# Kernel optimization log

Measured on AMD Instinct MI355X. Metric: run time of the kernel, lower is better.

## Reference

```python
import math
import jax, jax.numpy as jnp
import numpy as np

BSZ, SEQ, DIM = 2, 2048, 4096
N_HEADS, N_KV = 32, 8
HEAD_DIM = DIM // N_HEADS  # 128
N_REP = N_HEADS // N_KV    # 4
EPS = 1e-5
ROPE_THETA = 500000.0


def setup_inputs() -> dict:
    key = jax.random.key(0)
    ks = jax.random.split(key, 6)
    scale = 0.02
    x = jax.random.normal(ks[0], (BSZ, SEQ, DIM), dtype=jnp.float32)
    wq = jax.random.normal(ks[1], (N_HEADS * HEAD_DIM, DIM), dtype=jnp.float32) * scale
    wk = jax.random.normal(ks[2], (N_KV * HEAD_DIM, DIM), dtype=jnp.float32) * scale
    wv = jax.random.normal(ks[3], (N_KV * HEAD_DIM, DIM), dtype=jnp.float32) * scale
    wo = jax.random.normal(ks[4], (N_HEADS * HEAD_DIM, DIM), dtype=jnp.float32).T * scale  # [DIM, n_heads*hd] -> stored as [out,in]
    wo = jax.random.normal(ks[4], (DIM, N_HEADS * HEAD_DIM), dtype=jnp.float32) * scale
    # RoPE tables (real/imag parts of freqs_cis)
    inv_freq = 1.0 / (ROPE_THETA ** (jnp.arange(0, HEAD_DIM, 2, dtype=jnp.float32) / HEAD_DIM))
    angles = jnp.arange(SEQ, dtype=jnp.float32)[:, None] * inv_freq[None, :]  # [SEQ, HEAD_DIM//2]
    cos, sin = jnp.cos(angles), jnp.sin(angles)
    # causal additive mask
    neg_inf = jnp.finfo(jnp.float32).min
    mask = jnp.where(jnp.tril(jnp.ones((SEQ, SEQ), dtype=bool)), 0.0, neg_inf).astype(jnp.float32)
    return {"x": x, "wq": wq, "wk": wk, "wv": wv, "wo": wo,
            "cos": cos, "sin": sin, "mask": mask, "start_pos": 0}


def _apply_rope(t, cos, sin):
    # t: [b, s, h, hd]; pairs (even, odd) as in view_as_complex
    tf = t.astype(jnp.float32).reshape(*t.shape[:-1], HEAD_DIM // 2, 2)
    e, o = tf[..., 0], tf[..., 1]
    c = cos[None, :, None, :]
    s = sin[None, :, None, :]
    out = jnp.stack([e * c - o * s, e * s + o * c], axis=-1)
    return out.reshape(t.shape).astype(t.dtype)


def _rmsnorm(t):
    tf = t.astype(jnp.float32)
    return (tf * jax.lax.rsqrt(jnp.mean(tf * tf, axis=-1, keepdims=True) + EPS)).astype(t.dtype)


def reference(x, wq, wk, wv, wo, cos, sin, mask, start_pos):
    b, s, _ = x.shape
    xq = (x @ wq.T).reshape(b, s, N_HEADS, HEAD_DIM)
    xk = (x @ wk.T).reshape(b, s, N_KV, HEAD_DIM)
    xv = (x @ wv.T).reshape(b, s, N_KV, HEAD_DIM)
    xq = _apply_rope(xq, cos, sin)
    xk = _apply_rope(xk, cos, sin)
    xq = _rmsnorm(xq)
    xk = _rmsnorm(xk)
    # KV cache write/read with start_pos=0 over seqlen tokens is identity here.
    # GQA without repeat_interleave: q head h attends kv head h // N_REP
    q = xq.transpose(0, 2, 1, 3).reshape(b, N_KV, N_REP, s, HEAD_DIM)
    k = xk.transpose(0, 2, 1, 3)  # [b, n_kv, s, hd]
    v = xv.transpose(0, 2, 1, 3)
    scale = 1.0 / math.sqrt(HEAD_DIM)
    scores = jnp.einsum('bgrqd,bgkd->bgrqk', q, k) * scale + mask[None, None, None]
    probs = jax.nn.softmax(scores, axis=-1)
    out = jnp.einsum('bgrqk,bgkd->bgrqd', probs, v)
    out = out.reshape(b, N_HEADS, s, HEAD_DIM).transpose(0, 2, 1, 3).reshape(b, s, N_HEADS * HEAD_DIM)
    return out @ wo.T
```

## Files before the change

### kernel.cpp

```cpp
#include <hip/hip_runtime.h>
#include <hip/hip_bf16.h>
#include <stdint.h>

#define SEQ 2048
#define DIMSZ 4096
#define QKVN 6144

typedef __attribute__((ext_vector_type(8))) __bf16 bf16x8;
typedef __attribute__((ext_vector_type(4))) float f32x4;

static __device__ __forceinline__ void gld_lds16(const void* g, void* l) {
  __builtin_amdgcn_global_load_lds(
      (__attribute__((address_space(1))) void*)(g),
      (__attribute__((address_space(3))) void*)(l), 16, 0, 0);
}

__global__ __launch_bounds__(256) void k_cvt5(const float* __restrict__ x,
                                              const float* __restrict__ wq,
                                              const float* __restrict__ wk,
                                              const float* __restrict__ wv,
                                              const float* __restrict__ wo,
                                              __bf16* __restrict__ xb,
                                              __bf16* __restrict__ wqkvb,
                                              __bf16* __restrict__ wob) {
  long vid = (long)blockIdx.x * 256 + threadIdx.x;
  const long stride = (long)gridDim.x * 256;
  for (; vid < 7340032L; vid += stride) {
    const float* src; __bf16* dst; long off;
    if (vid < 2097152L)      { src = x;  dst = xb;                off = vid; }
    else if (vid < 4194304L) { src = wq; dst = wqkvb;             off = vid - 2097152L; }
    else if (vid < 4718592L) { src = wk; dst = wqkvb + 16777216L; off = vid - 4194304L; }
    else if (vid < 5242880L) { src = wv; dst = wqkvb + 20971520L; off = vid - 4718592L; }
    else                     { src = wo; dst = wob;               off = vid - 5242880L; }
    const long e = off * 8;
    float4 v0 = *(const float4*)(src + e);
    float4 v1 = *(const float4*)(src + e + 4);
    bf16x8 o;
    o[0] = (__bf16)v0.x; o[1] = (__bf16)v0.y; o[2] = (__bf16)v0.z; o[3] = (__bf16)v0.w;
    o[4] = (__bf16)v1.x; o[5] = (__bf16)v1.y; o[6] = (__bf16)v1.z; o[7] = (__bf16)v1.w;
    *(bf16x8*)(dst + e) = o;
  }
}

template <typename OutT>
__global__ __launch_bounds__(512) void k_gemm8p(const __bf16* __restrict__ A,
                                                const __bf16* __restrict__ B,
                                                OutT* __restrict__ C,
                                                int M, int N, int K) {
  __shared__ __align__(16) __bf16 As[2][2][128 * 64];
  __shared__ __align__(16) __bf16 Bs[2][2][128 * 64];
  const int t = threadIdx.x;
  const int l = t & 63;
  const int w = t >> 6;
  const int wm = w >> 2;
  const int wn = w & 3;
  const int lr = l & 15, lg = l >> 4;
  const int sw = lr & 7;
  const int bm = blockIdx.y, bn = blockIdx.x;

  const int srow = t >> 3;
  const int scol = ((t & 7) ^ (srow & 7)) << 3;
  const __bf16* pa0 = A + (size_t)(bm * 256 +   0 + srow) * K + scol;
  const __bf16* pa1 = A + (size_t)(bm * 256 +  64 + srow) * K + scol;
  const __bf16* pa2 = A + (size_t)(bm * 256 + 128 + srow) * K + scol;
  const __bf16* pa3 = A + (size_t)(bm * 256 + 192 + srow) * K + scol;
  const __bf16* pb0 = B + (size_t)(bn * 256 +   0 + srow) * K + scol;
  const __bf16* pb1 = B + (size_t)(bn * 256 +  64 + srow) * K + scol;
  const __bf16* pb2 = B + (size_t)(bn * 256 + 128 + srow) * K + scol;
  const __bf16* pb3 = B + (size_t)(bn * 256 + 192 + srow) * K + scol;
  const int ldst = t * 8;

#define SA0(buf, kc) { gld_lds16(pa0 + (kc), &As[buf][0][ldst]); gld_lds16(pa1 + (kc), &As[buf][0][4096 + ldst]); }
#define SA1(buf, kc) { gld_lds16(pa2 + (kc), &As[buf][1][ldst]); gld_lds16(pa3 + (kc), &As[buf][1][4096 + ldst]); }
#define SB0(buf, kc) { gld_lds16(pb0 + (kc), &Bs[buf][0][ldst]); gld_lds16(pb1 + (kc), &Bs[buf][0][4096 + ldst]); }
#define SB1(buf, kc) { gld_lds16(pb2 + (kc), &Bs[buf][1][ldst]); gld_lds16(pb3 + (kc), &Bs[buf][1][4096 + ldst]); }

  const int c0 = ((lg ^ sw) * 8);
  const int c1 = (((lg ^ sw) ^ 4) * 8);
  const int aRow = lr;
  const int bRow = (wn & 1) * 64 + lr;

#define RDA(mi0, cur)                                                          \
  _Pragma("unroll") for (int mi = 0; mi < 4; ++mi) {                           \
    a[mi][0] = *(const bf16x8*)&As[cur][wm][(((mi0) + mi) * 16 + aRow) * 64 + c0]; \
    a[mi][1] = *(const bf16x8*)&As[cur][wm][(((mi0) + mi) * 16 + aRow) * 64 + c1]; \
  }
#define RDB(bv, ni0, cur)                                                      \
  _Pragma("unroll") for (int ni = 0; ni < 2; ++ni) {                           \
    bv[ni][0] = *(const bf16x8*)&Bs[cur][wn >> 1][(((ni0) + ni) * 16 + bRow) * 64 + c0]; \
    bv[ni][1] = *(const bf16x8*)&Bs[cur][wn >> 1][(((ni0) + ni) * 16 + bRow) * 64 + c1]; \
  }
#define PHTOP()                                        \
  asm volatile("" ::: "memory");                       \
  __builtin_amdgcn_s_barrier();                        \
  asm volatile("s_waitcnt lgkmcnt(0)" ::: "memory");   \
  __builtin_amdgcn_s_setprio(1)
#define PHEND()                                        \
  __builtin_amdgcn_s_setprio(0);                       \
  asm volatile("" ::: "memory");                       \
  __builtin_amdgcn_s_barrier()
#define PHENDW()                                       \
  __builtin_amdgcn_s_setprio(0);                       \
  asm volatile("s_waitcnt vmcnt(8)" ::: "memory");     \
  __builtin_amdgcn_s_barrier()
#define MMA16(am0, bv, ni0)                                                    \
  _Pragma("unroll") for (int mi = 0; mi < 4; ++mi)                             \
  _Pragma("unroll") for (int ni = 0; ni < 2; ++ni)                             \
  _Pragma("unroll") for (int kk = 0; kk < 2; ++kk)                             \
    acc[(am0) + mi][(ni0) + ni] = __builtin_amdgcn_mfma_f32_16x16x32_bf16(     \
        a[mi][kk], bv[ni][kk], acc[(am0) + mi][(ni0) + ni], 0, 0, 0);

  f32x4 acc[8][4] = {};
  const int nt = K >> 6;
  const int niter = nt >> 1;

  {
    const int k1 = (nt > 1 ? 1 : 0) << 6;
    SB0(0, 0); SB1(0, 0); SA0(0, 0); SA1(0, 0);
    SB0(1, k1); SB1(1, k1); SA0(1, k1); SA1(1, k1);
  }
  asm volatile("s_waitcnt vmcnt(8)" ::: "memory");
  asm volatile("" ::: "memory");
  __builtin_amdgcn_s_barrier();
  asm volatile("" ::: "memory");

  for (int i = 0; i < niter; ++i) {
    const int k2 = (2 * i + 2 < nt ? 2 * i + 2 : nt - 1) << 6;
    const int k3 = (2 * i + 3 < nt ? 2 * i + 3 : nt - 1) << 6;
    bf16x8 a[4][2], b0[2][2], b1[2][2];

    RDA(0, 0); RDB(b0, 0, 0);
    PHTOP(); MMA16(0, b0, 0); PHEND();
    RDB(b1, 2, 0);
    PHTOP(); MMA16(0, b1, 2); PHEND();
    RDA(4, 0);
    SB0(0, k2); SB1(0, k2);
    PHTOP(); MMA16(4, b1, 2); PHEND();
    SA0(0, k2); SA1(0, k2);
    PHTOP(); MMA16(4, b0, 0); PHENDW();

    RDA(0, 1); RDB(b0, 0, 1);
    PHTOP(); MMA16(0, b0, 0); PHEND();
    RDB(b1, 2, 1);
    PHTOP(); MMA16(0, b1, 2); PHEND();
    RDA(4, 1);
    SB0(1, k3); SB1(1, k3);
    PHTOP(); MMA16(4, b1, 2); PHEND();
    SA0(1, k3); SA1(1, k3);
    PHTOP(); MMA16(4, b0, 0); PHENDW();
  }
#undef SA0
#undef SA1
#undef SB0
#undef SB1
#undef RDA
#undef RDB
#undef PHTOP
#undef PHEND
#undef PHENDW
#undef MMA16

  const int row0 = bm * 256 + wm * 128;
  const int col0 = bn * 256 + wn * 64;
#pragma unroll
  for (int mi = 0; mi < 8; ++mi)
#pragma unroll
    for (int ni = 0; ni < 4; ++ni)
#pragma unroll
      for (int r = 0; r < 4; ++r)
        C[(size_t)(row0 + mi * 16 + lg * 4 + r) * N + (col0 + ni * 16 + lr)] =
            (OutT)acc[mi][ni][r];
}

__global__ __launch_bounds__(256) void k_rope_norm(__bf16* __restrict__ qkv,
                                                   const float* __restrict__ cosT,
                                                   const float* __restrict__ sinT) {
  const int task = blockIdx.x * 4 + (threadIdx.x >> 6);
  const int l = threadIdx.x & 63;
  const int m = task / 40;
  const int h = task - m * 40;
  const int s = m & (SEQ - 1);
  const bool isQ = h < 32;
  const int col = isQ ? h * 128 : 4096 + (h - 32) * 128;
  __bf16* p = qkv + (size_t)m * QKVN + col + l * 2;
  float e = (float)p[0], o = (float)p[1];
  float c = cosT[s * 64 + l], sn = sinT[s * 64 + l];
  float e2 = e * c - o * sn;
  float o2 = e * sn + o * c;
  float ss = e2 * e2 + o2 * o2;
#pragma unroll
  for (int off = 32; off > 0; off >>= 1) ss += __shfl_xor(ss, off);
  float r = rsqrtf(ss * (1.0f / 128.0f) + 1e-5f);
  if (isQ) r *= 0.08838834764831845f;
  p[0] = (__bf16)(e2 * r);
  p[1] = (__bf16)(o2 * r);
}

__global__ __launch_bounds__(256) void k_transpose_v(const __bf16* __restrict__ qkv,
                                                     __bf16* __restrict__ vt) {
  __shared__ __bf16 tile[64][136];
  const int t = threadIdx.x;
  const int st = blockIdx.x, bg = blockIdx.y;
  const int b = bg >> 3, g = bg & 7;
  const int s0 = st * 64;
#pragma unroll
  for (int p = 0; p < 4; ++p) {
    int row = p * 16 + (t >> 4);
    int co = (t & 15) * 8;
    *(bf16x8*)&tile[row][co] =
        *(const bf16x8*)&qkv[(size_t)(b * SEQ + s0 + row) * QKVN + 5120 + g * 128 + co];
  }
  __syncthreads();
#pragma unroll
  for (int p = 0; p < 4; ++p) {
    int d = p * 32 + (t >> 3);
    int so = (t & 7) * 8;
    bf16x8 v;
#pragma unroll
    for (int j = 0; j < 8; ++j) v[j] = tile[so + j][d];
    *(bf16x8*)&vt[((size_t)bg * 128 + d) * SEQ + s0 + so] = v;
  }
}

__global__ __launch_bounds__(256) void k_flash(const __bf16* __restrict__ qkv,
                                               const __bf16* __restrict__ vt,
                                               __bf16* __restrict__ attno) {
  __shared__ __bf16 Ks[64 * 128];
  __shared__ __bf16 Vs[128 * 64];
  __shared__ __bf16 Ps[4][16 * 64];
  const int t = threadIdx.x, w = t >> 6, l = t & 63;
  const int lr = l & 15, lg = l >> 4;
  const int bh = blockIdx.y;
  const int b = bh >> 5, h = bh & 31, g = h >> 2;
  const int qt0 = blockIdx.x, qt1 = 31 - (int)blockIdx.x;

  const __bf16* kp = qkv + 4096 + (size_t)(b * SEQ + (t >> 4)) * QKVN + g * 128 +
                     (((t & 15) ^ ((t >> 4) & 7)) * 8);
  const __bf16* vp = vt + (size_t)(b * 8 + g) * 128 * SEQ + (size_t)(t >> 3) * SEQ +
                     (((t & 7) ^ ((t >> 3) & 7)) * 8);
  const int wbase = (t & ~63) * 8;
  const int sw = lr & 7;

  for (int pass = 0; pass < 2; ++pass) {
    const int qt = (pass == 0) ? qt0 : qt1;

    const __bf16* Qb = qkv + (size_t)(b * SEQ + qt * 64 + w * 16 + lr) * QKVN + h * 128;
    bf16x8 qf[4];
#pragma unroll
    for (int kk = 0; kk < 4; ++kk) qf[kk] = *(const bf16x8*)&Qb[kk * 32 + lg * 8];

    f32x4 oacc[8] = {};
    float mrow[4], lsum[4];
#pragma unroll
    for (int r = 0; r < 4; ++r) { mrow[r] = -1e30f; lsum[r] = 0.f; }

    for (int kt = 0; kt <= qt; ++kt) {
      const size_t kv0 = (size_t)kt * 64;
#pragma unroll
      for (int i = 0; i < 4; ++i)
        gld_lds16(kp + (kv0 + i * 16) * QKVN, &Ks[i * 2048 + wbase]);
#pragma unroll
      for (int i = 0; i < 4; ++i)
        gld_lds16(vp + (size_t)i * 32 * SEQ + kv0, &Vs[i * 2048 + wbase]);
      __syncthreads();

      f32x4 sc[4] = {};
      __builtin_amdgcn_s_setprio(1);
#pragma unroll
      for (int kk = 0; kk < 4; ++kk)
#pragma unroll
        for (int n = 0; n < 4; ++n) {
          bf16x8 kf = *(const bf16x8*)&Ks[(n * 16 + lr) * 128 + ((kk * 4 + lg) ^ sw) * 8];
          sc[n] = __builtin_amdgcn_mfma_f32_16x16x32_bf16(qf[kk], kf, sc[n], 0, 0, 0);
        }
      __builtin_amdgcn_s_setprio(0);

      if (kt == qt) {
#pragma unroll
        for (int n = 0; n < 4; ++n)
#pragma unroll
          for (int r = 0; r < 4; ++r)
            if (n * 16 + lr > w * 16 + lg * 4 + r) sc[n][r] = -1e30f;
      }

      float pml[4];
      float need = -1e30f;
#pragma unroll
      for (int r = 0; r < 4; ++r) {
        pml[r] = fmaxf(fmaxf(sc[0][r], sc[1][r]), fmaxf(sc[2][r], sc[3][r]));
        need = fmaxf(need, pml[r] - mrow[r]);
      }
      if (__all(need <= 8.0f)) {
#pragma unroll
        for (int r = 0; r < 4; ++r) {
          float ps = 0.f;
#pragma unroll
          for (int n = 0; n < 4; ++n) { sc[n][r] = __expf(sc[n][r] - mrow[r]); ps += sc[n][r]; }
#pragma unroll
          for (int off = 8; off > 0; off >>= 1) ps += __shfl_xor(ps, off);
          lsum[r] += ps;
        }
      } else {
#pragma unroll
        for (int r = 0; r < 4; ++r) {
          float pm = pml[r];
#pragma unroll
          for (int off = 8; off > 0; off >>= 1) pm = fmaxf(pm, __shfl_xor(pm, off));
          float mn = fmaxf(mrow[r], pm);
          float corr = __expf(mrow[r] - mn);
          mrow[r] = mn;
          float ps = 0.f;
#pragma unroll
          for (int n = 0; n < 4; ++n) { sc[n][r] = __expf(sc[n][r] - mn); ps += sc[n][r]; }
#pragma unroll
          for (int off = 8; off > 0; off >>= 1) ps += __shfl_xor(ps, off);
          lsum[r] = lsum[r] * corr + ps;
#pragma unroll
          for (int dn = 0; dn < 8; ++dn) oacc[dn][r] *= corr;
        }
      }

#pragma unroll
      for (int n = 0; n < 4; ++n)
#pragma unroll
        for (int r = 0; r < 4; ++r) {
          int row = lg * 4 + r;
          Ps[w][row * 64 + (((n * 2 + (lr >> 3)) ^ (row & 7)) * 8) + (lr & 7)] = (__bf16)sc[n][r];
        }

      __builtin_amdgcn_s_setprio(1);
#pragma unroll
      for (int ks = 0; ks < 2; ++ks) {
        bf16x8 pf = *(const bf16x8*)&Ps[w][lr * 64 + ((ks * 4 + lg) ^ sw) * 8];
#pragma unroll
        for (int dn = 0; dn < 8; ++dn) {
          bf16x8 vf = *(const bf16x8*)&Vs[(dn * 16 + lr) * 64 + ((ks * 4 + lg) ^ sw) * 8];
          oacc[dn] = __builtin_amdgcn_mfma_f32_16x16x32_bf16(pf, vf, oacc[dn], 0, 0, 0);
        }
      }
      __builtin_amdgcn_s_setprio(0);
      __syncthreads();
    }

    float inv[4];
#pragma unroll
    for (int r = 0; r < 4; ++r) inv[r] = __builtin_amdgcn_rcpf(lsum[r]);
    __bf16* Ob = attno + (size_t)(b * SEQ + qt * 64 + w * 16) * DIMSZ + h * 128;
#pragma unroll
    for (int dn = 0; dn < 8; ++dn)
#pragma unroll
      for (int r = 0; r < 4; ++r)
        Ob[(size_t)(lg * 4 + r) * DIMSZ + dn * 16 + lr] = (__bf16)(oacc[dn][r] * inv[r]);
  }
}

extern "C" void kernel_launch(void* const* d_in, const int* in_sizes, int n_in,
                              void* d_out, int out_size, void* d_ws, size_t ws_size,
                              hipStream_t stream) {
  const float* x    = (const float*)d_in[0];
  const float* wq   = (const float*)d_in[1];
  const float* wk   = (const float*)d_in[2];
  const float* wv   = (const float*)d_in[3];
  const float* wo   = (const float*)d_in[4];
  const float* cosT = (const float*)d_in[5];
  const float* sinT = (const float*)d_in[6];

  char* ws = (char*)d_ws;
  __bf16* xb    = (__bf16*)(ws);
  __bf16* wqkvb = (__bf16*)(ws + 33554432);
  __bf16* qkvb  = (__bf16*)(ws + 83886080);
  __bf16* wob   = (__bf16*)(ws + 134217728);
  __bf16* vt    = (__bf16*)(ws + 167772160);
  __bf16* attno = (__bf16*)(ws + 176160768);
  float* out = (float*)d_out;

  k_cvt5<<<4096, 256, 0, stream>>>(x, wq, wk, wv, wo, xb, wqkvb, wob);

  k_gemm8p<__bf16><<<dim3(24, 16), 512, 0, stream>>>(xb, wqkvb, qkvb, 4096, QKVN, 4096);
  k_rope_norm<<<40960, 256, 0, stream>>>(qkvb, cosT, sinT);
  k_transpose_v<<<dim3(32, 16), 256, 0, stream>>>(qkvb, vt);
  k_flash<<<dim3(16, 64), 256, 0, stream>>>(qkvb, vt, attno);
  k_gemm8p<float><<<dim3(16, 16), 512, 0, stream>>>(attno, wob, out, 4096, DIMSZ, 4096);
}
```

Baseline: 598.8 us.

## Add 128x256-tile triple-buffered GEMM for QKV projection

Introduces a new bf16 GEMM kernel with 128x256 output tiles and a three-stage LDS buffer ring, where global-to-LDS loads for A and B are interleaved with the two MFMA phases of each k-step. It replaces the previous 256x256 double-buffered kernel for the QKV projection, doubling the grid to 768 blocks for better CU occupancy and load balance on the device. The trade-off is smaller tiles, so less data reuse per block and more total global traffic, plus extra barrier synchronisation.

```diff
diff --git a/kernel.cpp b/kernel.cpp
--- a/kernel.cpp
+++ b/kernel.cpp
@@ -42,6 +42,130 @@
   }
 }
 
+__global__ __launch_bounds__(512) void k_gemm128x256(const __bf16* __restrict__ A,
+                                                     const __bf16* __restrict__ B,
+                                                     __bf16* __restrict__ C,
+                                                     int M, int N, int K) {
+  __shared__ __align__(16) __bf16 As[3][128 * 64];
+  __shared__ __align__(16) __bf16 Bs[3][256 * 64];
+  const int t = threadIdx.x;
+  const int l = t & 63;
+  const int w = t >> 6;
+  const int wm = w >> 2;
+  const int wn = w & 3;
+  const int lr = l & 15, lg = l >> 4;
+  const int sw = lr & 7;
+  const int bm = blockIdx.y, bn = blockIdx.x;
+
+  const int srow = t >> 3;
+  const int scol = ((t & 7) ^ (srow & 7)) << 3;
+  const __bf16* pa0 = A + (size_t)(bm * 128 +   0 + srow) * K + scol;
+  const __bf16* pa1 = A + (size_t)(bm * 128 +  64 + srow) * K + scol;
+  const __bf16* pb0 = B + (size_t)(bn * 256 +   0 + srow) * K + scol;
+  const __bf16* pb1 = B + (size_t)(bn * 256 +  64 + srow) * K + scol;
+  const __bf16* pb2 = B + (size_t)(bn * 256 + 128 + srow) * K + scol;
+  const __bf16* pb3 = B + (size_t)(bn * 256 + 192 + srow) * K + scol;
+  const int ldst = t * 8;
+
+#define SA(buf, kc) { gld_lds16(pa0 + (kc), &As[buf][ldst]);        \
+                      gld_lds16(pa1 + (kc), &As[buf][4096 + ldst]); }
+#define SB(buf, kc) { gld_lds16(pb0 + (kc), &Bs[buf][ldst]);        \
+                      gld_lds16(pb1 + (kc), &Bs[buf][4096 + ldst]); \
+                      gld_lds16(pb2 + (kc), &Bs[buf][8192 + ldst]); \
+                      gld_lds16(pb3 + (kc), &Bs[buf][12288 + ldst]); }
+
+  const int c0 = ((lg ^ sw) * 8);
+  const int c1 = (((lg ^ sw) ^ 4) * 8);
+  const int aBase = wm * 4096 + lr * 64;
+  const int bBase = wn * 4096 + lr * 64;
+
+#define PHTOP()                                        \
+  asm volatile("" ::: "memory");                       \
+  __builtin_amdgcn_s_barrier();                        \
+  asm volatile("s_waitcnt lgkmcnt(0)" ::: "memory");   \
+  __builtin_amdgcn_s_setprio(1)
+#define PHEND()                                        \
+  __builtin_amdgcn_s_setprio(0);                       \
+  asm volatile("" ::: "memory");                       \
+  __builtin_amdgcn_s_barrier()
+#define PHENDW()                                       \
+  __builtin_amdgcn_s_setprio(0);                       \
+  asm volatile("s_waitcnt vmcnt(6)" ::: "memory");     \
+  __builtin_amdgcn_s_barrier()
+
+  f32x4 acc[4][4] = {};
+  const int nt = K >> 6;
+
+  SA(0, 0); SB(0, 0);
+  SA(1, 64); SB(1, 64);
+  asm volatile("s_waitcnt vmcnt(6)" ::: "memory");
+  asm volatile("" ::: "memory");
+  __builtin_amdgcn_s_barrier();
+  asm volatile("" ::: "memory");
+
+  int bu = 0, bu2 = 2;
+  for (int U = 0; U < nt; ++U) {
+    const int kc = (U + 2 < nt ? U + 2 : nt - 1) << 6;
+    bf16x8 a[4][2], b[2][2];
+
+#pragma unroll
+    for (int mi = 0; mi < 4; ++mi) {
+      a[mi][0] = *(const bf16x8*)&As[bu][aBase + mi * 1024 + c0];
+      a[mi][1] = *(const bf16x8*)&As[bu][aBase + mi * 1024 + c1];
+    }
+#pragma unroll
+    for (int ni = 0; ni < 2; ++ni) {
+      b[ni][0] = *(const bf16x8*)&Bs[bu][bBase + ni * 1024 + c0];
+      b[ni][1] = *(const bf16x8*)&Bs[bu][bBase + ni * 1024 + c1];
+    }
+    SA(bu2, kc);
+    PHTOP();
+#pragma unroll
+    for (int mi = 0; mi < 4; ++mi)
+#pragma unroll
+      for (int ni = 0; ni < 2; ++ni)
+#pragma unroll
+        for (int kk = 0; kk < 2; ++kk)
+          acc[mi][ni] = __builtin_amdgcn_mfma_f32_16x16x32_bf16(a[mi][kk], b[ni][kk], acc[mi][ni], 0, 0, 0);
+    PHEND();
+
+#pragma unroll
+    for (int ni = 0; ni < 2; ++ni) {
+      b[ni][0] = *(const bf16x8*)&Bs[bu][bBase + (ni + 2) * 1024 + c0];
+      b[ni][1] = *(const bf16x8*)&Bs[bu][bBase + (ni + 2) * 1024 + c1];
+    }
+    SB(bu2, kc);
+    PHTOP();
+#pragma unroll
+    for (int mi = 0; mi < 4; ++mi)
+#pragma unroll
+      for (int ni = 0; ni < 2; ++ni)
+#pragma unroll
+        for (int kk = 0; kk < 2; ++kk)
+          acc[mi][ni + 2] = __builtin_amdgcn_mfma_f32_16x16x32_bf16(a[mi][kk], b[ni][kk], acc[mi][ni + 2], 0, 0, 0);
+    PHENDW();
+
+    bu = (bu == 2) ? 0 : bu + 1;
+    bu2 = (bu2 == 2) ? 0 : bu2 + 1;
+  }
+#undef SA
+#undef SB
+#undef PHTOP
+#undef PHEND
+#undef PHENDW
+
+  const int row0 = bm * 128 + wm * 64;
+  const int col0 = bn * 256 + wn * 64;
+#pragma unroll
+  for (int mi = 0; mi < 4; ++mi)
+#pragma unroll
+    for (int ni = 0; ni < 4; ++ni)
+#pragma unroll
+      for (int r = 0; r < 4; ++r)
+        C[(size_t)(row0 + mi * 16 + lg * 4 + r) * N + (col0 + ni * 16 + lr)] =
+            (__bf16)acc[mi][ni][r];
+}
+
 template <typename OutT>
 __global__ __launch_bounds__(512) void k_gemm8p(const __bf16* __restrict__ A,
                                                 const __bf16* __restrict__ B,
@@ -376,7 +500,7 @@
 
   k_cvt5<<<4096, 256, 0, stream>>>(x, wq, wk, wv, wo, xb, wqkvb, wob);
 
-  k_gemm8p<__bf16><<<dim3(24, 16), 512, 0, stream>>>(xb, wqkvb, qkvb, 4096, QKVN, 4096);
+  k_gemm128x256<<<dim3(24, 32), 512, 0, stream>>>(xb, wqkvb, qkvb, 4096, QKVN, 4096);
   k_rope_norm<<<40960, 256, 0, stream>>>(qkvb, cosT, sinT);
   k_transpose_v<<<dim3(32, 16), 256, 0, stream>>>(qkvb, vt);
   k_flash<<<dim3(16, 64), 256, 0, stream>>>(qkvb, vt, attno);
```

Measured after the change: 586.4 us, median of 2. -2.1%, faster.

## Use 256x384 tile GEMM with K=32 stages for QKV projection

Applied to the files above, without the earlier changes.

Adds a new bf16 GEMM kernel for the QKV projection that uses a 256x384 block tile with a 32-wide K step and a double-buffered LDS stage loaded via direct global-to-LDS copies. Each wave accumulates a 128x96 sub-tile, which raises arithmetic intensity per LDS read. The grid becomes 16x16 blocks, exactly 256 tiles, so each CU gets one tile with fewer wave quantization tails. In exchange, register pressure rises from the 48 accumulator tiles per lane, and the short K step means more barriers per unit of work.

```diff
diff --git a/kernel.cpp b/kernel.cpp
--- a/kernel.cpp
+++ b/kernel.cpp
@@ -42,6 +42,89 @@
   }
 }
 
+__global__ __launch_bounds__(512, 2) void k_gemm1(const __bf16* __restrict__ A,
+                                                  const __bf16* __restrict__ B,
+                                                  __bf16* __restrict__ C,
+                                                  int M, int N, int K) {
+  __shared__ __align__(16) __bf16 As[2][256 * 32];
+  __shared__ __align__(16) __bf16 Bs[2][384 * 32];
+  const int t = threadIdx.x;
+  const int l = t & 63;
+  const int w = t >> 6;
+  const int wm = w >> 2;
+  const int wn = w & 3;
+  const int lr = l & 15, lg = l >> 4;
+  const int rsw = (lr >> 1) & 3;
+  const int bm = blockIdx.y, bn = blockIdx.x;
+
+  const int srow = t >> 2;
+  const int scol = (((t & 3) ^ ((t >> 3) & 3)) << 3);
+  const __bf16* pa0 = A + (size_t)(bm * 256 +   0 + srow) * K + scol;
+  const __bf16* pa1 = A + (size_t)(bm * 256 + 128 + srow) * K + scol;
+  const __bf16* pb0 = B + (size_t)(bn * 384 +   0 + srow) * K + scol;
+  const __bf16* pb1 = B + (size_t)(bn * 384 + 128 + srow) * K + scol;
+  const __bf16* pb2 = B + (size_t)(bn * 384 + 256 + srow) * K + scol;
+  const int ldst = t * 8;
+
+#define STAGE(buf, kc) {                               \
+    gld_lds16(pa0 + (kc), &As[buf][ldst]);             \
+    gld_lds16(pa1 + (kc), &As[buf][4096 + ldst]);      \
+    gld_lds16(pb0 + (kc), &Bs[buf][ldst]);             \
+    gld_lds16(pb1 + (kc), &Bs[buf][4096 + ldst]);      \
+    gld_lds16(pb2 + (kc), &Bs[buf][8192 + ldst]); }
+
+  const int cc = ((lg ^ rsw) * 8);
+  const int aBase = (wm * 128 + lr) * 32 + cc;
+  const int bBase = (wn * 96 + lr) * 32 + cc;
+
+  f32x4 acc[8][6] = {};
+  const int nt = K >> 5;
+
+  STAGE(0, 0);
+  __syncthreads();
+
+  for (int U = 0; U < nt; ++U) {
+    const int cur = U & 1;
+    const int kc = (U + 1 < nt ? U + 1 : nt - 1) << 5;
+    STAGE(cur ^ 1, kc);
+
+    bf16x8 b[6], a[4];
+#pragma unroll
+    for (int ni = 0; ni < 6; ++ni)
+      b[ni] = *(const bf16x8*)&Bs[cur][bBase + ni * 512];
+#pragma unroll
+    for (int mi = 0; mi < 4; ++mi)
+      a[mi] = *(const bf16x8*)&As[cur][aBase + mi * 512];
+#pragma unroll
+    for (int mi = 0; mi < 4; ++mi)
+#pragma unroll
+      for (int ni = 0; ni < 6; ++ni)
+        acc[mi][ni] = __builtin_amdgcn_mfma_f32_16x16x32_bf16(a[mi], b[ni], acc[mi][ni], 0, 0, 0);
+#pragma unroll
+    for (int mi = 0; mi < 4; ++mi)
+      a[mi] = *(const bf16x8*)&As[cur][aBase + (mi + 4) * 512];
+#pragma unroll
+    for (int mi = 0; mi < 4; ++mi)
+#pragma unroll
+      for (int ni = 0; ni < 6; ++ni)
+        acc[mi + 4][ni] = __builtin_amdgcn_mfma_f32_16x16x32_bf16(a[mi], b[ni], acc[mi + 4][ni], 0, 0, 0);
+
+    __syncthreads();
+  }
+#undef STAGE
+
+  const int row0 = bm * 256 + wm * 128;
+  const int col0 = bn * 384 + wn * 96;
+#pragma unroll
+  for (int mi = 0; mi < 8; ++mi)
+#pragma unroll
+    for (int ni = 0; ni < 6; ++ni)
+#pragma unroll
+      for (int r = 0; r < 4; ++r)
+        C[(size_t)(row0 + mi * 16 + lg * 4 + r) * N + (col0 + ni * 16 + lr)] =
+            (__bf16)acc[mi][ni][r];
+}
+
 template <typename OutT>
 __global__ __launch_bounds__(512) void k_gemm8p(const __bf16* __restrict__ A,
                                                 const __bf16* __restrict__ B,
@@ -376,7 +459,7 @@
 
   k_cvt5<<<4096, 256, 0, stream>>>(x, wq, wk, wv, wo, xb, wqkvb, wob);
 
-  k_gemm8p<__bf16><<<dim3(24, 16), 512, 0, stream>>>(xb, wqkvb, qkvb, 4096, QKVN, 4096);
+  k_gemm1<<<dim3(16, 16), 512, 0, stream>>>(xb, wqkvb, qkvb, 4096, QKVN, 4096);
   k_rope_norm<<<40960, 256, 0, stream>>>(qkvb, cosT, sinT);
   k_transpose_v<<<dim3(32, 16), 256, 0, stream>>>(qkvb, vt);
   k_flash<<<dim3(16, 64), 256, 0, stream>>>(qkvb, vt, attno);
```

Result: no change. 609.1 us (+1.7%).
